# Kernel tuning notes

Measured on AMD Instinct MI355X. Metric: run time of the kernel, lower is better.

Reference implementation:

```python
import jax, jax.numpy as jnp
import numpy as np
from jax import lax

A_PLUS = 0.01
A_MINUS = 0.01
TAU_PLUS = 20.0
TAU_MINUS = 20.0
W_MAX = 1.0
W_MIN = 0.0

B, T, PRE_N, POST_N = 16, 128, 2048, 2048


def setup_inputs() -> dict:
    key = jax.random.key(0)
    k1, k2, k3 = jax.random.split(key, 3)
    weights = jax.random.uniform(k1, (POST_N, PRE_N), dtype=jnp.float32)
    pre_spikes = jax.random.uniform(k2, (B, T, PRE_N), dtype=jnp.float32)
    post_spikes = jax.random.uniform(k3, (B, T, POST_N), dtype=jnp.float32)
    return {"weights": weights, "pre_spikes": pre_spikes,
            "post_spikes": post_spikes, "dt": 1}


def compute_trace(spikes, tau, dt):
    # Faithful to torch loop: trace[:,0,:] = 0; trace[t] = decay*trace[t-1] + spikes[t] for t>=1
    decay = jnp.exp(jnp.float32(-dt / tau))
    s_tb = jnp.swapaxes(spikes, 0, 1)  # [T, B, N]
    init = jnp.zeros_like(s_tb[0])

    def step(carry, s_t):
        tr = decay * carry + s_t
        return tr, tr

    _, tr = lax.scan(step, init, s_tb[1:])          # [T-1, B, N]
    tr = jnp.concatenate([init[None], tr], axis=0)  # [T, B, N]
    return jnp.swapaxes(tr, 0, 1)                   # [B, T, N]


def reference(weights, pre_spikes, post_spikes, dt):
    batch = pre_spikes.shape[0]
    pre_trace = compute_trace(pre_spikes, TAU_PLUS, dt)
    post_trace = compute_trace(post_spikes, TAU_MINUS, dt)

    # sum over t of mean over batch of outer products -> single contraction over (b, t)
    # ltp[q,p] = A_plus * sum_t mean_b post_spikes[b,t,q] * pre_trace[b,t,p]
    ltp = A_PLUS * jnp.einsum('btq,btp->qp', post_spikes, pre_trace) / batch
    # ltd[q,p] = -A_minus * sum_t mean_b post_trace[b,t,q] * pre_spikes[b,t,p]
    ltd = -A_MINUS * jnp.einsum('btq,btp->qp', post_trace, pre_spikes) / batch

    # softbound weight dependence (constant in t, distributes over the sum)
    w_factor = (W_MAX - weights) * (weights - W_MIN) / ((W_MAX - W_MIN) / 2) ** 2
    delta_w = w_factor * (ltp + ltd)
    return delta_w
```

## Files before the change

### kernel.cpp

```cpp
#include <hip/hip_runtime.h>
#include <hip/hip_bf16.h>


typedef __attribute__((ext_vector_type(8))) short bf16x8;
typedef __attribute__((ext_vector_type(4))) float f32x4;

#define GN 2048
#define KTOT 2048
#define A_SCALE (0.01f / 16.0f)
#define FST 68
#define ZST 66

#define GLOAD_LDS16(gp, lp) \
    __builtin_amdgcn_global_load_lds((const __attribute__((address_space(1))) void*)(gp), \
                                     (__attribute__((address_space(3))) void*)(lp), 16, 0, 0)

__device__ __forceinline__ unsigned bf16bits(float x) {
    __hip_bfloat16 h = __float2bfloat16(x);
    return (unsigned)*(unsigned short*)&h;
}

__global__ __launch_bounds__(256, 4) void trace_kernel(
    const float* __restrict__ pre,
    const float* __restrict__ post,
    const int* __restrict__ dtp,
    __hip_bfloat16* __restrict__ AT,
    __hip_bfloat16* __restrict__ BT)
{
    __shared__ float fbuf[128 * FST];
    __hip_bfloat16* zbuf = (__hip_bfloat16*)fbuf;

    const int tid = threadIdx.x;
    const int w   = tid >> 6;
    const int l   = tid & 63;
    const int nq  = tid & 15;
    const int tl  = tid >> 4;
    const int n0  = blockIdx.x * 64;
    const int b   = blockIdx.y;
    const int a   = blockIdx.z;

    int di = dtp[0];
    float dtf = (di > 0 && di < 1000000) ? (float)di : *(const float*)dtp;
    const float decay = __expf(-dtf / 20.0f);

    if (a == 0) {
        #pragma unroll
        for (int pass = 0; pass < 8; ++pass) {
            const int t = pass * 16 + tl;
            float4 v = *(const float4*)&post[((size_t)b * 128 + t) * GN + n0 + 4 * nq];
            uint2 pk;
            pk.x = bf16bits(v.x) | (bf16bits(v.y) << 16);
            pk.y = bf16bits(v.z) | (bf16bits(v.w) << 16);
            *(uint2*)&zbuf[t * ZST + 4 * nq] = pk;
        }
        __syncthreads();
    } else {
        #pragma unroll
        for (int pass = 0; pass < 8; ++pass) {
            const int t = pass * 16 + tl;
            float4 v = *(const float4*)&pre[((size_t)b * 128 + t) * GN + n0 + 4 * nq];
            *(float4*)&fbuf[t * FST + 4 * nq] = v;
        }
        __syncthreads();

        const int t0 = 32 * w;
        float carry = 0.0f;
        #pragma unroll 8
        for (int t = 1; t < t0; ++t)
            carry = decay * carry + fbuf[t * FST + l];
        float z[32];
        #pragma unroll
        for (int j = 0; j < 32; ++j) {
            const int t = t0 + j;
            if (t >= 1) carry = decay * carry + fbuf[t * FST + l];
            z[j] = carry;
        }
        float bc = 0.0f;
        #pragma unroll 8
        for (int t = 127; t >= t0 + 32; --t)
            bc = decay * bc + fbuf[t * FST + l];
        #pragma unroll
        for (int j = 31; j >= 0; --j) {
            const int t = t0 + j;
            bc = decay * bc + fbuf[t * FST + l];
            if (t >= 1) z[j] -= bc;
        }
        __syncthreads();
        #pragma unroll
        for (int j = 0; j < 32; ++j)
            zbuf[(t0 + j) * ZST + l] = __float2bfloat16(z[j]);
        __syncthreads();
    }

    __hip_bfloat16* dst = (a == 0) ? AT : BT;
    #pragma unroll
    for (int j = 0; j < 4; ++j) {
        const int c  = tid + 256 * j;
        const int n  = c >> 4;
        const int tc = c & 15;
        unsigned int vv[8];
        #pragma unroll
        for (int i = 0; i < 8; ++i)
            vv[i] = *(const unsigned short*)&zbuf[(8 * tc + i) * ZST + n];
        uint4 pk;
        pk.x = vv[0] | (vv[1] << 16);
        pk.y = vv[2] | (vv[3] << 16);
        pk.z = vv[4] | (vv[5] << 16);
        pk.w = vv[6] | (vv[7] << 16);
        *(uint4*)(dst + (size_t)(n0 + n) * KTOT + b * 128 + tc * 8) = pk;
    }
}

__global__ __launch_bounds__(512, 4) void stdp_gemm(
    const __hip_bfloat16* __restrict__ AT,
    const __hip_bfloat16* __restrict__ BT,
    const float* __restrict__ W,
    float* __restrict__ out)
{
    __shared__ alignas(16) char smem[73728];

    const int tid  = threadIdx.x;
    const int lane = tid & 63;
    const int wv8  = tid >> 6;
    const int wr   = wv8 >> 1;
    const int wc   = wv8 & 1;
    const int RM   = blockIdx.y * 128;
    const int CN   = blockIdx.x * 64;
    const int l15  = lane & 15;
    const int quad = lane >> 4;

    const int cS   = wv8 * 64 + lane;
    const int rS   = cS >> 3;
    const int sS   = cS & 7;
    const int kc0  = sS ^ (rS & 7);
    const int kc1  = sS ^ ((rS + 64) & 7);
    const __hip_bfloat16* srcA0 = AT + (size_t)(RM + rS)      * KTOT + kc0 * 8;
    const __hip_bfloat16* srcA1 = AT + (size_t)(RM + rS + 64) * KTOT + kc1 * 8;
    const __hip_bfloat16* srcB  = BT + (size_t)(CN + rS)      * KTOT + kc0 * 8;
    const int dS = wv8 * 1024;

#define STAGE(BUF, kstep) do {                                   \
        char* bb_ = (BUF);                                       \
        const int ke_ = (kstep) * 64;                            \
        GLOAD_LDS16(srcA0 + ke_, bb_ + dS);                      \
        GLOAD_LDS16(srcA1 + ke_, bb_ + 8192 + dS);               \
        GLOAD_LDS16(srcB  + ke_, bb_ + 16384 + dS);              \
    } while (0)

    const int mr0 = wr * 32 + l15;
    const int mr1 = mr0 + 16;
    const int nr0 = wc * 32 + l15;
    const int nr1 = nr0 + 16;

    f32x4 acc00 = {}, acc01 = {}, acc10 = {}, acc11 = {};

#define COMPUTE(BUF) do {                                                         \
        const __hip_bfloat16* Ab_ = (const __hip_bfloat16*)(BUF);                 \
        const __hip_bfloat16* Bb_ = (const __hip_bfloat16*)((BUF) + 16384);       \
        _Pragma("unroll")                                                         \
        for (int kk_ = 0; kk_ < 2; ++kk_) {                                       \
            const int jg_ = kk_ * 4 + quad;                                       \
            bf16x8 a0_ = *(const bf16x8*)(Ab_ + mr0 * 64 + ((jg_ ^ (mr0 & 7)) * 8)); \
            bf16x8 a1_ = *(const bf16x8*)(Ab_ + mr1 * 64 + ((jg_ ^ (mr1 & 7)) * 8)); \
            bf16x8 b0_ = *(const bf16x8*)(Bb_ + nr0 * 64 + ((jg_ ^ (nr0 & 7)) * 8)); \
            bf16x8 b1_ = *(const bf16x8*)(Bb_ + nr1 * 64 + ((jg_ ^ (nr1 & 7)) * 8)); \
            acc00 = __builtin_amdgcn_mfma_f32_16x16x32_bf16(a0_, b0_, acc00, 0, 0, 0); \
            acc01 = __builtin_amdgcn_mfma_f32_16x16x32_bf16(a0_, b1_, acc01, 0, 0, 0); \
            acc10 = __builtin_amdgcn_mfma_f32_16x16x32_bf16(a1_, b0_, acc10, 0, 0, 0); \
            acc11 = __builtin_amdgcn_mfma_f32_16x16x32_bf16(a1_, b1_, acc11, 0, 0, 0); \
        }                                                                         \
    } while (0)

#define WAITBAR(N) do {                                          \
        asm volatile("s_waitcnt vmcnt(" #N ")" ::: "memory");    \
        __builtin_amdgcn_s_barrier();                            \
        __builtin_amdgcn_sched_barrier(0);                       \
    } while (0)

    char* B0 = smem;
    char* B1 = smem + 24576;
    char* B2 = smem + 49152;

    STAGE(B0, 0);
    STAGE(B1, 1);
    WAITBAR(3);

    for (int hb = 0; hb < 30; hb += 3) {
        STAGE(B2, hb + 2); COMPUTE(B0); WAITBAR(3);
        STAGE(B0, hb + 3); COMPUTE(B1); WAITBAR(3);
        STAGE(B1, hb + 4); COMPUTE(B2); WAITBAR(3);
    }
    COMPUTE(B0);
    WAITBAR(0);
    COMPUTE(B1);

#undef STAGE
#undef COMPUTE
#undef WAITBAR

    #pragma unroll
    for (int i = 0; i < 2; ++i) {
        #pragma unroll
        for (int j = 0; j < 2; ++j) {
            const f32x4 a = (i == 0) ? (j == 0 ? acc00 : acc01)
                                     : (j == 0 ? acc10 : acc11);
            const int p = CN + wc * 32 + j * 16 + l15;
            #pragma unroll
            for (int r = 0; r < 4; ++r) {
                const int q = RM + wr * 32 + i * 16 + quad * 4 + r;
                const float w  = W[(size_t)q * GN + p];
                const float wf = 4.0f * w * (1.0f - w);
                out[(size_t)q * GN + p] = wf * A_SCALE * a[r];
            }
        }
    }
}

extern "C" void kernel_launch(void* const* d_in, const int* in_sizes, int n_in,
                              void* d_out, int out_size, void* d_ws, size_t ws_size,
                              hipStream_t stream) {
    const float* W    = (const float*)d_in[0];
    const float* pre  = (const float*)d_in[1];
    const float* post = (const float*)d_in[2];
    const int*   dt   = (const int*)d_in[3];
    float* out = (float*)d_out;

    __hip_bfloat16* AT = (__hip_bfloat16*)d_ws;
    __hip_bfloat16* BT = AT + (size_t)GN * KTOT;

    trace_kernel<<<dim3(32, 16, 2), 256, 0, stream>>>(pre, post, dt, AT, BT);
    stdp_gemm<<<dim3(32, 16), 512, 0, stream>>>(AT, BT, W, out);
}
```

Before: 117.7 us.

## Halve GEMM block to four waves, each computing a 64x32 tile

The GEMM block drops from 8 waves to 4, with each wave now covering 64 rows by 32 columns (8 MFMA accumulators instead of 4). Each thread issues 6 global-to-LDS loads per stage instead of 3, and the wait counts change to match. The aim is more MFMA work per LDS fragment read (B fragments reused across four A fragments) and fewer waves per block, at the cost of more registers per thread and less latency hiding from wave count.

```diff
diff --git a/kernel.cpp b/kernel.cpp
--- a/kernel.cpp
+++ b/kernel.cpp
@@ -111,7 +111,7 @@
     }
 }
 
-__global__ __launch_bounds__(512, 4) void stdp_gemm(
+__global__ __launch_bounds__(256) void stdp_gemm(
     const __hip_bfloat16* __restrict__ AT,
     const __hip_bfloat16* __restrict__ BT,
     const float* __restrict__ W,
@@ -121,38 +121,43 @@
 
     const int tid  = threadIdx.x;
     const int lane = tid & 63;
-    const int wv8  = tid >> 6;
-    const int wr   = wv8 >> 1;
-    const int wc   = wv8 & 1;
+    const int wv   = tid >> 6;
+    const int wr   = wv >> 1;
+    const int wc   = wv & 1;
     const int RM   = blockIdx.y * 128;
     const int CN   = blockIdx.x * 64;
     const int l15  = lane & 15;
     const int quad = lane >> 4;
 
-    const int cS   = wv8 * 64 + lane;
-    const int rS   = cS >> 3;
-    const int sS   = cS & 7;
-    const int kc0  = sS ^ (rS & 7);
-    const int kc1  = sS ^ ((rS + 64) & 7);
-    const __hip_bfloat16* srcA0 = AT + (size_t)(RM + rS)      * KTOT + kc0 * 8;
-    const __hip_bfloat16* srcA1 = AT + (size_t)(RM + rS + 64) * KTOT + kc1 * 8;
-    const __hip_bfloat16* srcB  = BT + (size_t)(CN + rS)      * KTOT + kc0 * 8;
-    const int dS = wv8 * 1024;
+    const int rS = (wv << 3) + (lane >> 3);
+    const int kc = (lane & 7) ^ ((lane >> 3) & 7);
+    const __hip_bfloat16* sA0 = AT + (size_t)(RM + rS)      * KTOT + kc * 8;
+    const __hip_bfloat16* sA1 = AT + (size_t)(RM + rS + 32) * KTOT + kc * 8;
+    const __hip_bfloat16* sA2 = AT + (size_t)(RM + rS + 64) * KTOT + kc * 8;
+    const __hip_bfloat16* sA3 = AT + (size_t)(RM + rS + 96) * KTOT + kc * 8;
+    const __hip_bfloat16* sB0 = BT + (size_t)(CN + rS)      * KTOT + kc * 8;
+    const __hip_bfloat16* sB1 = BT + (size_t)(CN + rS + 32) * KTOT + kc * 8;
+    const int dS = wv * 1024;
 
 #define STAGE(BUF, kstep) do {                                   \
         char* bb_ = (BUF);                                       \
         const int ke_ = (kstep) * 64;                            \
-        GLOAD_LDS16(srcA0 + ke_, bb_ + dS);                      \
-        GLOAD_LDS16(srcA1 + ke_, bb_ + 8192 + dS);               \
-        GLOAD_LDS16(srcB  + ke_, bb_ + 16384 + dS);              \
+        GLOAD_LDS16(sA0 + ke_, bb_ + dS);                        \
+        GLOAD_LDS16(sA1 + ke_, bb_ + 4096 + dS);                 \
+        GLOAD_LDS16(sA2 + ke_, bb_ + 8192 + dS);                 \
+        GLOAD_LDS16(sA3 + ke_, bb_ + 12288 + dS);                \
+        GLOAD_LDS16(sB0 + ke_, bb_ + 16384 + dS);                \
+        GLOAD_LDS16(sB1 + ke_, bb_ + 20480 + dS);                \
     } while (0)
 
-    const int mr0 = wr * 32 + l15;
+    const int mr0 = wr * 64 + l15;
     const int mr1 = mr0 + 16;
+    const int mr2 = mr0 + 32;
+    const int mr3 = mr0 + 48;
     const int nr0 = wc * 32 + l15;
     const int nr1 = nr0 + 16;
 
-    f32x4 acc00 = {}, acc01 = {}, acc10 = {}, acc11 = {};
+    f32x4 acc[4][2] = {};
 
 #define COMPUTE(BUF) do {                                                         \
         const __hip_bfloat16* Ab_ = (const __hip_bfloat16*)(BUF);                 \
@@ -160,14 +165,20 @@
         _Pragma("unroll")                                                         \
         for (int kk_ = 0; kk_ < 2; ++kk_) {                                       \
             const int jg_ = kk_ * 4 + quad;                                       \
+            bf16x8 b0_ = *(const bf16x8*)(Bb_ + nr0 * 64 + ((jg_ ^ (nr0 & 7)) * 8)); \
+            bf16x8 b1_ = *(const bf16x8*)(Bb_ + nr1 * 64 + ((jg_ ^ (nr1 & 7)) * 8)); \
             bf16x8 a0_ = *(const bf16x8*)(Ab_ + mr0 * 64 + ((jg_ ^ (mr0 & 7)) * 8)); \
             bf16x8 a1_ = *(const bf16x8*)(Ab_ + mr1 * 64 + ((jg_ ^ (mr1 & 7)) * 8)); \
-            bf16x8 b0_ = *(const bf16x8*)(Bb_ + nr0 * 64 + ((jg_ ^ (nr0 & 7)) * 8)); \
-            bf16x8 b1_ = *(const bf16x8*)(Bb_ + nr1 * 64 + ((jg_ ^ (nr1 & 7)) * 8)); \
-            acc00 = __builtin_amdgcn_mfma_f32_16x16x32_bf16(a0_, b0_, acc00, 0, 0, 0); \
-            acc01 = __builtin_amdgcn_mfma_f32_16x16x32_bf16(a0_, b1_, acc01, 0, 0, 0); \
-            acc10 = __builtin_amdgcn_mfma_f32_16x16x32_bf16(a1_, b0_, acc10, 0, 0, 0); \
-            acc11 = __builtin_amdgcn_mfma_f32_16x16x32_bf16(a1_, b1_, acc11, 0, 0, 0); \
+            bf16x8 a2_ = *(const bf16x8*)(Ab_ + mr2 * 64 + ((jg_ ^ (mr2 & 7)) * 8)); \
+            bf16x8 a3_ = *(const bf16x8*)(Ab_ + mr3 * 64 + ((jg_ ^ (mr3 & 7)) * 8)); \
+            acc[0][0] = __builtin_amdgcn_mfma_f32_16x16x32_bf16(a0_, b0_, acc[0][0], 0, 0, 0); \
+            acc[0][1] = __builtin_amdgcn_mfma_f32_16x16x32_bf16(a0_, b1_, acc[0][1], 0, 0, 0); \
+            acc[1][0] = __builtin_amdgcn_mfma_f32_16x16x32_bf16(a1_, b0_, acc[1][0], 0, 0, 0); \
+            acc[1][1] = __builtin_amdgcn_mfma_f32_16x16x32_bf16(a1_, b1_, acc[1][1], 0, 0, 0); \
+            acc[2][0] = __builtin_amdgcn_mfma_f32_16x16x32_bf16(a2_, b0_, acc[2][0], 0, 0, 0); \
+            acc[2][1] = __builtin_amdgcn_mfma_f32_16x16x32_bf16(a2_, b1_, acc[2][1], 0, 0, 0); \
+            acc[3][0] = __builtin_amdgcn_mfma_f32_16x16x32_bf16(a3_, b0_, acc[3][0], 0, 0, 0); \
+            acc[3][1] = __builtin_amdgcn_mfma_f32_16x16x32_bf16(a3_, b1_, acc[3][1], 0, 0, 0); \
         }                                                                         \
     } while (0)
 
@@ -183,12 +194,12 @@
 
     STAGE(B0, 0);
     STAGE(B1, 1);
-    WAITBAR(3);
+    WAITBAR(6);
 
     for (int hb = 0; hb < 30; hb += 3) {
-        STAGE(B2, hb + 2); COMPUTE(B0); WAITBAR(3);
-        STAGE(B0, hb + 3); COMPUTE(B1); WAITBAR(3);
-        STAGE(B1, hb + 4); COMPUTE(B2); WAITBAR(3);
+        STAGE(B2, hb + 2); COMPUTE(B0); WAITBAR(6);
+        STAGE(B0, hb + 3); COMPUTE(B1); WAITBAR(6);
+        STAGE(B1, hb + 4); COMPUTE(B2); WAITBAR(6);
     }
     COMPUTE(B0);
     WAITBAR(0);
@@ -199,18 +210,16 @@
 #undef WAITBAR
 
     #pragma unroll
-    for (int i = 0; i < 2; ++i) {
-        #pragma unroll
-        for (int j = 0; j < 2; ++j) {
-            const f32x4 a = (i == 0) ? (j == 0 ? acc00 : acc01)
-                                     : (j == 0 ? acc10 : acc11);
-            const int p = CN + wc * 32 + j * 16 + l15;
+    for (int i = 0; i < 4; ++i) {
+        #pragma unroll
+        for (int r = 0; r < 4; ++r) {
+            const int q = RM + wr * 64 + i * 16 + quad * 4 + r;
             #pragma unroll
-            for (int r = 0; r < 4; ++r) {
-                const int q = RM + wr * 32 + i * 16 + quad * 4 + r;
+            for (int j = 0; j < 2; ++j) {
+                const int p = CN + wc * 32 + j * 16 + l15;
                 const float w  = W[(size_t)q * GN + p];
                 const float wf = 4.0f * w * (1.0f - w);
-                out[(size_t)q * GN + p] = wf * A_SCALE * a[r];
+                out[(size_t)q * GN + p] = wf * A_SCALE * acc[i][j][r];
             }
         }
     }
@@ -229,5 +238,5 @@
     __hip_bfloat16* BT = AT + (size_t)GN * KTOT;
 
     trace_kernel<<<dim3(32, 16, 2), 256, 0, stream>>>(pre, post, dt, AT, BT);
-    stdp_gemm<<<dim3(32, 16), 512, 0, stream>>>(AT, BT, W, out);
-}
+    stdp_gemm<<<dim3(32, 16), 256, 0, stream>>>(AT, BT, W, out);
+}
```

New measurement: 119.9 us. No clear change (+1.9%).
